# Kernel optimization log

Measured on AMD Instinct MI355X. Metric: run time of the kernel, lower is better.

Reference implementation:

```python
import jax, jax.numpy as jnp
import numpy as np

DIM = 1024
HEADS = 16
HEAD_DIM = DIM // HEADS
T_MAX = 128
V = 12
T = 128
B = 4
N = V * T + 1  # 1537, includes cls token


def setup_inputs() -> dict:
    key = jax.random.key(0)
    ks = jax.random.split(key, 9)
    s = 0.02
    return {
        "x": jax.random.normal(ks[0], (B, N, DIM), dtype=jnp.float32),
        "qkv_w": jax.random.normal(ks[1], (3 * DIM, DIM), dtype=jnp.float32) * s,
        "in_proj_w": jax.random.normal(ks[2], (3 * DIM, DIM), dtype=jnp.float32) * s,
        "in_proj_b": jax.random.normal(ks[3], (3 * DIM,), dtype=jnp.float32) * s,
        "out_proj_w": jax.random.normal(ks[4], (DIM, DIM), dtype=jnp.float32) * s,
        "out_proj_b": jax.random.normal(ks[5], (DIM,), dtype=jnp.float32) * s,
        "proj_w": jax.random.normal(ks[6], (DIM, DIM), dtype=jnp.float32) * s,
        "proj_b": jax.random.normal(ks[7], (DIM,), dtype=jnp.float32) * s,
        "ids_restore": jax.random.randint(ks[8], (B, V * T), 0, 1000000, dtype=jnp.int64),
        "V_input": V,
        "T_input": T,
    }


def _rope_tables(dtype):
    # theta_d = 10000^{-2d/head_dim}, positions 0..T_max (position 0 is the cls slot)
    theta = 10000.0 ** (-jnp.arange(0, HEAD_DIM, 2, dtype=dtype) / HEAD_DIM)  # (hd/2,)
    pos = jnp.arange(1 + T_MAX, dtype=dtype)
    ang = pos[:, None] * theta[None, :]  # (1+T_max, hd/2)
    return jnp.cos(ang), jnp.sin(ang)


def _rotate(t, cos_g, sin_g):
    # t: (B, N, D); cos_g/sin_g: (B, N-1, 1, hd/2) gathered per non-cls token
    b, n, d = t.shape
    t4 = t.reshape(b, n, HEADS, HEAD_DIM)
    re, im = t4[..., ::2], t4[..., 1::2]  # even/odd interleave -> (B,N,H,hd/2)
    # cls token uses position 0: cos=1, sin=0 -> identity rotation, halves concatenated
    cls = jnp.concatenate([re[:, :1], im[:, :1]], axis=-1)  # (B,1,H,hd)
    rest = jnp.concatenate(
        [re[:, 1:] * cos_g - im[:, 1:] * sin_g,
         re[:, 1:] * sin_g + im[:, 1:] * cos_g], axis=-1)  # (B,N-1,H,hd)
    return jnp.concatenate([cls, rest], axis=1).reshape(b, n, d)


def reference(x, qkv_w, in_proj_w, in_proj_b, out_proj_w, out_proj_b,
              proj_w, proj_b, ids_restore, V_input, T_input):
    b, n, d = x.shape
    # --- qkv projection (no bias) ---
    qkv = jnp.einsum('bnd,ed->bne', x, qkv_w)  # (B,N,3D)
    q, k, v = jnp.split(qkv, 3, axis=-1)
    # --- temporal RoPE with ids_restore-based gather ---
    cos_t, sin_t = _rope_tables(x.dtype)  # (1+T_max, hd/2)
    ids_shuffle = jnp.argsort(ids_restore, axis=1)[:, : n - 1] % V_input  # (B,N-1)
    cos_g = cos_t[ids_shuffle + 1][:, :, None, :]  # gather from cos[:,1:] slice
    sin_g = sin_t[ids_shuffle + 1][:, :, None, :]
    q = _rotate(q, cos_g, sin_g)
    k = _rotate(k, cos_g, sin_g)
    # --- nn.MultiheadAttention (batch_first, no mask, eval) ---
    wq, wk, wv = in_proj_w[:d], in_proj_w[d:2 * d], in_proj_w[2 * d:]
    bq, bk, bv = in_proj_b[:d], in_proj_b[d:2 * d], in_proj_b[2 * d:]
    qp = (jnp.einsum('bnd,ed->bne', q, wq) + bq).reshape(b, n, HEADS, HEAD_DIM)
    kp = (jnp.einsum('bnd,ed->bne', k, wk) + bk).reshape(b, n, HEADS, HEAD_DIM)
    vp = (jnp.einsum('bnd,ed->bne', v, wv) + bv).reshape(b, n, HEADS, HEAD_DIM)
    scale = 1.0 / jnp.sqrt(jnp.asarray(HEAD_DIM, x.dtype))
    scores = jnp.einsum('bqhe,bkhe->bhqk', qp * scale, kp)  # (B,H,N,N)
    attn = jax.nn.softmax(scores, axis=-1)
    ctx = jnp.einsum('bhqk,bkhe->bqhe', attn, vp).reshape(b, n, d)
    mha_out = jnp.einsum('bnd,ed->bne', ctx, out_proj_w) + out_proj_b
    # --- final projection ---
    out = jnp.einsum('bnd,ed->bne', mha_out, proj_w) + proj_b
    return out


if __name__ == '__main__':
    inp = setup_inputs()
    print(reference(**inp).shape)
```

## Files before the change

kernel.cpp:

```cpp
#include <hip/hip_runtime.h>
#include <math.h>

#define B_ 4
#define NTOK 1537
#define NH 16
#define NROWS 6148
#define RPAD 6272
#define KDIM 1024
#define NKT 49

typedef __attribute__((ext_vector_type(8))) short short8;
typedef __attribute__((ext_vector_type(4))) float f32x4;
typedef __attribute__((ext_vector_type(16))) float f32x16;
typedef __attribute__((ext_vector_type(4))) unsigned short ushort4v;
typedef __attribute__((ext_vector_type(4))) unsigned int uint4v;
typedef __attribute__((ext_vector_type(2))) unsigned int uint2v;

__device__ __forceinline__ float bf2f(unsigned short u){
  unsigned int x = ((unsigned int)u) << 16;
  return __uint_as_float(x);
}
__device__ __forceinline__ unsigned short f2bf(float f){
  unsigned int x = __float_as_uint(f);
  x += 0x7fff + ((x >> 16) & 1);
  return (unsigned short)(x >> 16);
}
__device__ __forceinline__ unsigned int pack_bf16(float lo, float hi){
  return (unsigned int)f2bf(lo) | ((unsigned int)f2bf(hi) << 16);
}
__device__ __forceinline__ unsigned int pack_bf16_fast(float lo, float hi){
  unsigned int ue = __float_as_uint(lo) + 0x8000u;
  unsigned int uo = __float_as_uint(hi) + 0x8000u;
  return __builtin_amdgcn_perm(uo, ue, 0x07060302u);
}
__device__ __forceinline__ float fast_exp2(float x){
  return __builtin_amdgcn_exp2f(x);
}
__device__ __forceinline__ uint2v permswap(unsigned int a, unsigned int b){
  return __builtin_amdgcn_permlane32_swap(a, b, false, false);
}
__device__ __forceinline__ void gload_lds16(const void* g, void* l){
  __builtin_amdgcn_global_load_lds((const __attribute__((address_space(1))) unsigned int*)g,
                                   (__attribute__((address_space(3))) unsigned int*)l, 16, 0, 0);
}
__device__ __forceinline__ f32x4 mfma16(short8 a, short8 b, f32x4 c){
  return __builtin_amdgcn_mfma_f32_16x16x32_bf16(a, b, c, 0, 0, 0);
}
__device__ __forceinline__ f32x16 mfma32(short8 a, short8 b, f32x16 c){
  return __builtin_amdgcn_mfma_f32_32x32x16_bf16(a, b, c, 0, 0, 0);
}

__global__ __launch_bounds__(256) void cvt_w_kernel(const float* __restrict__ src,
                                                    unsigned short* __restrict__ dst, int n){
  int i = (blockIdx.x*256 + threadIdx.x)*4;
  if (i >= n) return;
  f32x4 v = *(const f32x4*)(src + i);
  ushort4v o;
  #pragma unroll
  for (int j=0;j<4;j++) o[j] = f2bf(v[j]);
  *(ushort4v*)(dst + i) = o;
}

__global__ __launch_bounds__(256) void cvt_wT_kernel(const float* __restrict__ src, int r0,
                                                     unsigned short* __restrict__ dst){
  __shared__ float Tl[64][65];
  int ct = blockIdx.x, rt = blockIdx.y;
  int t = threadIdx.x;
  int i = t >> 4, j4 = (t & 15) * 4;
  #pragma unroll
  for (int s = 0; s < 4; s++){
    int rl = s*16 + i;
    f32x4 v = *(const f32x4*)(src + (size_t)(r0 + rt*64 + rl)*1024 + ct*64 + j4);
    Tl[rl][j4+0]=v[0]; Tl[rl][j4+1]=v[1]; Tl[rl][j4+2]=v[2]; Tl[rl][j4+3]=v[3];
  }
  __syncthreads();
  #pragma unroll
  for (int s = 0; s < 4; s++){
    int cl = s*16 + i;
    ushort4v o;
    #pragma unroll
    for (int k=0;k<4;k++) o[k] = f2bf(Tl[j4+k][cl]);
    *(ushort4v*)(dst + (size_t)(ct*64 + cl)*1024 + rt*64 + j4) = o;
  }
}

__global__ __launch_bounds__(256) void cvt_x_kernel(const float* __restrict__ x,
                                                    unsigned short* __restrict__ xb){
  size_t i = ((size_t)blockIdx.x*256 + threadIdx.x)*4;
  if (i >= (size_t)RPAD*KDIM) return;
  size_t row = i >> 10;
  ushort4v o;
  if (row < NROWS){
    f32x4 v = *(const f32x4*)(x + i);
    #pragma unroll
    for (int j=0;j<4;j++) o[j] = f2bf(v[j]);
  } else {
    o = (ushort4v)0;
  }
  *(ushort4v*)(xb + i) = o;
}

__global__ __launch_bounds__(64) void fuse_bias_kernel(const float* __restrict__ pw,
    const float* __restrict__ opb, const float* __restrict__ pb, float* __restrict__ bf){
  int c = blockIdx.x;
  int t = threadIdx.x;
  const float* row = pw + (size_t)c*1024;
  float s = 0.f;
  #pragma unroll
  for (int e=0; e<16; e++) s += row[t + e*64] * opb[t + e*64];
  #pragma unroll
  for (int off=1; off<64; off<<=1) s += __shfl_xor(s, off);
  if (t == 0) bf[c] = s + pb[c];
}

__global__ void rope_tables_kernel(float* __restrict__ ct, float* __restrict__ st){
  int i = threadIdx.x;
  if (i >= 13*32) return;
  int p = i >> 5, j = i & 31;
  float th = powf(10000.f, -(float)j * (1.f/32.f));
  float ang = (float)p * th;
  ct[i] = cosf(ang);
  st[i] = sinf(ang);
}

__global__ __launch_bounds__(256) void argsort_kernel(const int* __restrict__ ids,
                                                      int* __restrict__ postab){
  __shared__ int vals[1536];
  int b = blockIdx.x;
  const int* src = ids + b*1536;
  for (int i=threadIdx.x; i<1536; i+=256) vals[i] = src[i];
  __syncthreads();
  int i = blockIdx.y*256 + threadIdx.x;
  int v = vals[i];
  int rank = 0;
  for (int j=0;j<1536;j++){
    int u = vals[j];
    rank += (u < v) || (u == v && j < i);
  }
  postab[b*1536 + rank] = (i % 12) + 1;
}

__global__ __launch_bounds__(256) void rope_kernel(unsigned short* __restrict__ qkv,
                                                   const int* __restrict__ postab,
                                                   const float* __restrict__ ct,
                                                   const float* __restrict__ st){
  int idx = blockIdx.x*256 + threadIdx.x;
  if (idx >= B_*NTOK*NH) return;
  int h = idx & 15;
  int bn = idx >> 4;
  int b = bn / NTOK;
  int n = bn - b*NTOK;
  unsigned short* rowp = qkv + (size_t)bn*2048;
  int pos = (n == 0) ? 0 : postab[b*1536 + (n-1)];
  const float* cr = ct + pos*32;
  const float* sr = st + pos*32;
  #pragma unroll
  for (int part=0; part<2; part++){
    unsigned short* p = rowp + part*1024 + h*64;
    uint4v vv[8];
    #pragma unroll
    for (int i=0;i<8;i++) vv[i] = ((const uint4v*)p)[i];
    unsigned short* tp = (unsigned short*)vv;
    unsigned short ov[64];
    if (n == 0){
      #pragma unroll
      for (int j=0;j<32;j++){ ov[j] = tp[2*j]; ov[32+j] = tp[2*j+1]; }
    } else {
      #pragma unroll
      for (int j=0;j<32;j++){
        float re = bf2f(tp[2*j]), im = bf2f(tp[2*j+1]);
        float c = cr[j], s = sr[j];
        ov[j]    = f2bf(re*c - im*s);
        ov[32+j] = f2bf(re*s + im*c);
      }
    }
    #pragma unroll
    for (int i=0;i<8;i++) ((uint4v*)p)[i] = ((const uint4v*)ov)[i];
  }
}

__device__ __forceinline__ void gemm_body(const unsigned short* __restrict__ A, int lda,
    const unsigned short* __restrict__ W,
    const float* __restrict__ bias, float scale,
    unsigned short* __restrict__ outb, float* __restrict__ outf, int ldo, int mvalid,
    int rowBase, int colBase)
{
  __shared__ alignas(16) unsigned short At[128][32];
  __shared__ alignas(16) unsigned short Bt[128][32];
  int t = threadIdx.x, w = t >> 6, lane = t & 63;
  int g = lane >> 4, l15 = lane & 15;
  int rb = (w >> 1) * 64, cb = (w & 1) * 64;
  f32x4 acc[4][4];
  #pragma unroll
  for (int m=0;m<4;m++)
    #pragma unroll
    for (int n=0;n<4;n++) acc[m][n] = 0.f;
  int srow = lane >> 2;
  int scol = (lane & 3) * 8;
  for (int kb = 0; kb < KDIM; kb += 32){
    __syncthreads();
    #pragma unroll
    for (int i=0;i<2;i++){
      int rr = i*64 + w*16 + srow;
      gload_lds16(A + (size_t)(rowBase + rr)*lda + kb + scol, &At[i*64 + w*16][0]);
      gload_lds16(W + (size_t)(colBase + rr)*KDIM + kb + scol, &Bt[i*64 + w*16][0]);
    }
    __syncthreads();
    short8 af[4], bf[4];
    #pragma unroll
    for (int m=0;m<4;m++) af[m] = *(const short8*)&At[rb + m*16 + l15][g*8];
    #pragma unroll
    for (int n=0;n<4;n++) bf[n] = *(const short8*)&Bt[cb + n*16 + l15][g*8];
    #pragma unroll
    for (int m=0;m<4;m++)
      #pragma unroll
      for (int n=0;n<4;n++)
        acc[m][n] = mfma16(af[m], bf[n], acc[m][n]);
  }
  #pragma unroll
  for (int m=0;m<4;m++)
    #pragma unroll
    for (int n=0;n<4;n++){
      int col = colBase + cb + n*16 + l15;
      float bv = bias ? bias[col] : 0.f;
      #pragma unroll
      for (int r=0;r<4;r++){
        int row = rowBase + rb + m*16 + g*4 + r;
        if (row < mvalid){
          float v = (acc[m][n][r] + bv) * scale;
          if (outf) outf[(size_t)row*ldo + col] = v;
          else      outb[(size_t)row*ldo + col] = f2bf(v);
        }
      }
    }
}

__global__ __launch_bounds__(256) void gemm_kernel(const unsigned short* __restrict__ A, int lda,
    const unsigned short* __restrict__ W,
    const float* __restrict__ bias, float scale,
    unsigned short* __restrict__ outb, float* __restrict__ outf, int ldo, int mvalid)
{
  gemm_body(A, lda, W, bias, scale, outb, outf, ldo, mvalid,
            blockIdx.x*128, blockIdx.y*128);
}

__global__ __launch_bounds__(256) void gemm_qkv_kernel(const unsigned short* __restrict__ xb,
    const unsigned short* __restrict__ qkvwb, const unsigned short* __restrict__ Wvb,
    const float* __restrict__ ipb, unsigned short* __restrict__ qkb,
    unsigned short* __restrict__ vpb)
{
  int cy = blockIdx.y;
  bool isV = cy >= 16;
  const unsigned short* W = isV ? Wvb : qkvwb;
  const float* bias = isV ? ipb + 2048 : nullptr;
  unsigned short* outb = isV ? vpb : qkb;
  int ldo = isV ? 1024 : 2048;
  int colBase = (isV ? cy - 16 : cy) * 128;
  gemm_body(xb, 1024, W, bias, 1.f, outb, nullptr, ldo, NROWS,
            blockIdx.x*128, colBase);
}

__global__ __launch_bounds__(256) void gemm_inproj_kernel(const unsigned short* __restrict__ qkb,
    const unsigned short* __restrict__ ipwb, const float* __restrict__ ipb,
    unsigned short* __restrict__ qpb, unsigned short* __restrict__ kpb)
{
  int z = blockIdx.z;
  const unsigned short* A = qkb + z*1024;
  const unsigned short* W = ipwb + (size_t)z*1024*1024;
  const float* bias = ipb + z*1024;
  float scale = (z == 0) ? 0.125f*1.44269504f : 1.f;
  unsigned short* outb = (z == 0) ? qpb : kpb;
  gemm_body(A, 2048, W, bias, scale, outb, nullptr, 1024, NROWS,
            blockIdx.x*128, blockIdx.y*128);
}

__global__ __launch_bounds__(256) void gemm_prep_kernel(const unsigned short* __restrict__ pwb,
    const unsigned short* __restrict__ opwT, const unsigned short* __restrict__ wv,
    const unsigned short* __restrict__ qkvwTv,
    unsigned short* __restrict__ Wfb, unsigned short* __restrict__ Wvb)
{
  int z = blockIdx.z;
  const unsigned short* A = z ? wv : pwb;
  const unsigned short* W = z ? qkvwTv : opwT;
  unsigned short* outb = z ? Wvb : Wfb;
  gemm_body(A, 1024, W, nullptr, 1.f, outb, nullptr, 1024, 1024,
            blockIdx.x*128, blockIdx.y*128);
}

__global__ __launch_bounds__(256) void frag_kernel(const unsigned short* __restrict__ kp,
    const unsigned short* __restrict__ vp,
    unsigned short* __restrict__ kf, unsigned short* __restrict__ vf){
  __shared__ alignas(16) unsigned short Tl[32][72];
  int bh = blockIdx.x, kt = blockIdx.y;
  int b = bh >> 4, h = bh & 15;
  int t = threadIdx.x;
  if (blockIdx.z == 0){
    int lane = t & 63, c = t >> 6;
    int l31 = lane & 31, hh = lane >> 5;
    int key = kt*32 + l31; if (key > NTOK-1) key = NTOK-1;
    uint4v v = *(const uint4v*)(kp + (size_t)(b*NTOK + key)*KDIM + h*64 + c*16 + hh*8);
    *(uint4v*)(kf + (size_t)(bh*NKT + kt)*2048 + c*512 + lane*8) = v;
  } else {
    {
      int r = t >> 3, ch = t & 7;
      int key = kt*32 + r;
      uint4v v;
      if (key < NTOK){
        v = *(const uint4v*)(vp + (size_t)(b*NTOK + key)*KDIM + h*64 + ch*8);
      } else v = (uint4v)0;
      *(uint4v*)&Tl[r][ch*8] = v;
    }
    __syncthreads();
    {
      int lane = t & 63, w = t >> 6;
      int l31 = lane & 31, hh = lane >> 5;
      int dblk = w >> 1, c = w & 1;
      unsigned short ov[8];
      #pragma unroll
      for (int j=0;j<8;j++) ov[j] = Tl[c*16 + hh*8 + j][dblk*32 + l31];
      *(uint4v*)(vf + (size_t)(bh*NKT + kt)*2048 + w*512 + lane*8) = *(const uint4v*)ov;
    }
  }
}

__global__ __launch_bounds__(256) void attn_kernel(const unsigned short* __restrict__ qp,
    const unsigned short* __restrict__ kf, const unsigned short* __restrict__ vf,
    unsigned short* __restrict__ ctx)
{
  int bh = blockIdx.x;
  int qt = blockIdx.y;
  int b = bh >> 4, hd = bh & 15;
  int t = threadIdx.x, w = t >> 6, lane = t & 63;
  int l31 = lane & 31, hh = lane >> 5;
  int qrow = qt*128 + w*32 + l31;
  int qcl = qrow > NTOK-1 ? NTOK-1 : qrow;
  const unsigned short* qb = qp + (((size_t)(b*NTOK + qcl)*NH + hd) << 6) + hh*8;
  short8 qf[4];
  #pragma unroll
  for (int c=0;c<4;c++) qf[c] = *(const short8*)(qb + c*16);
  const unsigned short* kfb = kf + (size_t)(bh*NKT)*2048 + lane*8;
  const unsigned short* vfb = vf + (size_t)(bh*NKT)*2048 + lane*8;
  float m_ = -3e38f, l_ = 0.f;
  f32x16 o0 = 0.f, o1 = 0.f;

  auto soft_pv = [&](f32x16 cc, short8 va00, short8 va01, short8 va10, short8 va11){
    float t0 = fmaxf(fmaxf(cc[0],cc[1]), fmaxf(cc[2],cc[3]));
    float t1 = fmaxf(fmaxf(cc[4],cc[5]), fmaxf(cc[6],cc[7]));
    float t2 = fmaxf(fmaxf(cc[8],cc[9]), fmaxf(cc[10],cc[11]));
    float t3 = fmaxf(fmaxf(cc[12],cc[13]), fmaxf(cc[14],cc[15]));
    float mx = fmaxf(fmaxf(t0,t1), fmaxf(t2,t3));
    {
      uint2v pr = permswap(__float_as_uint(mx), __float_as_uint(mx));
      mx = fmaxf(__uint_as_float(pr[0]), __uint_as_float(pr[1]));
    }
    if (!__all(mx <= m_ + 11.5f)){
      float mn = fmaxf(m_, mx);
      float al = fast_exp2(m_ - mn);
      m_ = mn;
      l_ *= al;
      #pragma unroll
      for (int i=0;i<16;i++){ o0[i] *= al; o1[i] *= al; }
    }
    float p[16], rs = 0.f;
    #pragma unroll
    for (int i=0;i<16;i++){ p[i] = fast_exp2(cc[i] - m_); }
    #pragma unroll
    for (int i=0;i<16;i++) rs += p[i];
    l_ += rs;
    unsigned int W[8];
    #pragma unroll
    for (int wd=0; wd<8; wd++) W[wd] = pack_bf16_fast(p[2*wd], p[2*wd+1]);
    uint2v e0 = permswap(W[0], W[2]);
    uint2v e1 = permswap(W[1], W[3]);
    uint2v e2 = permswap(W[4], W[6]);
    uint2v e3 = permswap(W[5], W[7]);
    uint4v u0, u1;
    u0[0]=e0[0]; u0[1]=e1[0]; u0[2]=e0[1]; u0[3]=e1[1];
    u1[0]=e2[0]; u1[1]=e3[0]; u1[2]=e2[1]; u1[3]=e3[1];
    short8 pb0, pb1;
    __builtin_memcpy(&pb0, &u0, 16);
    __builtin_memcpy(&pb1, &u1, 16);
    o0 = mfma32(va00, pb0, o0);
    o0 = mfma32(va01, pb1, o0);
    o1 = mfma32(va10, pb0, o1);
    o1 = mfma32(va11, pb1, o1);
  };

  short8 ka[4];
  #pragma unroll
  for (int c=0;c<4;c++) ka[c] = *(const short8*)(kfb + c*512);
  f32x16 cc = 0.f;
  cc = mfma32(ka[0], qf[0], cc);
  cc = mfma32(ka[1], qf[1], cc);
  cc = mfma32(ka[2], qf[2], cc);
  cc = mfma32(ka[3], qf[3], cc);
  #pragma unroll
  for (int c=0;c<4;c++) ka[c] = *(const short8*)(kfb + 2048 + c*512);

  for (int kt=0; kt<48; ++kt){
    const unsigned short* vB = vfb + (size_t)kt*2048;
    short8 va00 = *(const short8*)(vB);
    short8 va01 = *(const short8*)(vB + 512);
    short8 va10 = *(const short8*)(vB + 1024);
    short8 va11 = *(const short8*)(vB + 1536);
    f32x16 cn = 0.f;
    cn = mfma32(ka[0], qf[0], cn);
    cn = mfma32(ka[1], qf[1], cn);
    cn = mfma32(ka[2], qf[2], cn);
    cn = mfma32(ka[3], qf[3], cn);
    int ktn = kt+2 < NKT-1 ? kt+2 : NKT-1;
    const unsigned short* kB = kfb + (size_t)ktn*2048;
    #pragma unroll
    for (int c=0;c<4;c++) ka[c] = *(const short8*)(kB + c*512);
    soft_pv(cc, va00, va01, va10, va11);
    cc = cn;
  }
  {
    const unsigned short* vB = vfb + (size_t)48*2048;
    short8 va00 = *(const short8*)(vB);
    short8 va01 = *(const short8*)(vB + 512);
    short8 va10 = *(const short8*)(vB + 1024);
    short8 va11 = *(const short8*)(vB + 1536);
    #pragma unroll
    for (int i=0;i<16;i++) cc[i] = (i == 0 && hh == 0) ? cc[i] : -1e30f;
    soft_pv(cc, va00, va01, va10, va11);
  }
  {
    uint2v pr = permswap(__float_as_uint(l_), __float_as_uint(l_));
    l_ = __uint_as_float(pr[0]) + __uint_as_float(pr[1]);
  }
  if (qrow < NTOK){
    float inv = 1.f / l_;
    unsigned short* cb = ctx + (((size_t)(b*NTOK + qrow)*NH + hd) << 6) + 4*hh;
    #pragma unroll
    for (int s=0;s<4;s++){
      uint2v u;
      u[0] = pack_bf16(o0[4*s]*inv,   o0[4*s+1]*inv);
      u[1] = pack_bf16(o0[4*s+2]*inv, o0[4*s+3]*inv);
      *(uint2v*)(cb + 8*s) = u;
    }
    #pragma unroll
    for (int s=0;s<4;s++){
      uint2v u;
      u[0] = pack_bf16(o1[4*s]*inv,   o1[4*s+1]*inv);
      u[1] = pack_bf16(o1[4*s+2]*inv, o1[4*s+3]*inv);
      *(uint2v*)(cb + 32 + 8*s) = u;
    }
  }
}

extern "C" void kernel_launch(void* const* d_in, const int* in_sizes, int n_in,
                              void* d_out, int out_size, void* d_ws, size_t ws_size,
                              hipStream_t stream)
{
  const float* x    = (const float*)d_in[0];
  const float* qkvw = (const float*)d_in[1];
  const float* ipw  = (const float*)d_in[2];
  const float* ipb  = (const float*)d_in[3];
  const float* opw  = (const float*)d_in[4];
  const float* opb  = (const float*)d_in[5];
  const float* pw   = (const float*)d_in[6];
  const float* pb   = (const float*)d_in[7];
  const int*   ids  = (const int*)d_in[8];
  float* out = (float*)d_out;

  char* p = (char*)d_ws;
  auto alloc = [&](size_t bytes)->char* {
    char* r = p; p += (bytes + 255) & ~(size_t)255; return r;
  };
  unsigned short* xb     = (unsigned short*)alloc((size_t)RPAD*1024*2);
  unsigned short* qkvwb  = (unsigned short*)alloc((size_t)2048*1024*2);
  unsigned short* ipwb   = (unsigned short*)alloc((size_t)3072*1024*2);
  unsigned short* pwb    = (unsigned short*)alloc((size_t)1024*1024*2);
  unsigned short* opwT   = (unsigned short*)alloc((size_t)1024*1024*2);
  unsigned short* qkvwTv = (unsigned short*)alloc((size_t)1024*1024*2);
  unsigned short* Wfb    = (unsigned short*)alloc((size_t)1024*1024*2);
  unsigned short* Wvb    = (unsigned short*)alloc((size_t)1024*1024*2);
  float*          bfb    = (float*)alloc(1024*4);
  unsigned short* qkb    = (unsigned short*)alloc((size_t)RPAD*2048*2);
  unsigned short* qpb    = (unsigned short*)alloc((size_t)RPAD*1024*2);
  unsigned short* kpb    = (unsigned short*)alloc((size_t)RPAD*1024*2);
  unsigned short* vpb    = (unsigned short*)alloc((size_t)RPAD*1024*2);
  unsigned short* ctxb   = (unsigned short*)alloc((size_t)RPAD*1024*2);
  int*   postab = (int*)alloc((size_t)B_*1536*4);
  float* ctab   = (float*)alloc(13*32*4);
  float* stab   = (float*)alloc(13*32*4);
  unsigned short* vfb = xb;
  unsigned short* kfb = qkb;

  cvt_w_kernel<<<2048, 256, 0, stream>>>(qkvw, qkvwb, 2048*1024);
  cvt_w_kernel<<<3072, 256, 0, stream>>>(ipw,  ipwb,  3072*1024);
  cvt_w_kernel<<<1024, 256, 0, stream>>>(pw,   pwb,   1024*1024);
  cvt_wT_kernel<<<dim3(16,16), 256, 0, stream>>>(opw,  0,    opwT);
  cvt_wT_kernel<<<dim3(16,16), 256, 0, stream>>>(qkvw, 2048, qkvwTv);
  cvt_x_kernel<<<RPAD, 256, 0, stream>>>(x, xb);
  rope_tables_kernel<<<1, 512, 0, stream>>>(ctab, stab);
  argsort_kernel<<<dim3(B_, 6), 256, 0, stream>>>(ids, postab);

  gemm_prep_kernel<<<dim3(8, 8, 2), 256, 0, stream>>>(pwb, opwT, ipwb + (size_t)2048*1024,
                                                      qkvwTv, Wfb, Wvb);
  fuse_bias_kernel<<<1024, 64, 0, stream>>>(pw, opb, pb, bfb);

  gemm_qkv_kernel<<<dim3(RPAD/128, 24), 256, 0, stream>>>(xb, qkvwb, Wvb, ipb, qkb, vpb);
  rope_kernel<<<(B_*NTOK*NH + 255)/256, 256, 0, stream>>>(qkb, postab, ctab, stab);
  gemm_inproj_kernel<<<dim3(RPAD/128, 8, 2), 256, 0, stream>>>(qkb, ipwb, ipb, qpb, kpb);
  frag_kernel<<<dim3(B_*NH, NKT, 2), 256, 0, stream>>>(kpb, vpb, kfb, vfb);
  attn_kernel<<<dim3(B_*NH, 13), 256, 0, stream>>>(qpb, kfb, vfb, ctxb);
  gemm_kernel<<<dim3(RPAD/128, 8), 256, 0, stream>>>(ctxb, 1024, Wfb, bfb, 1.f,
                                                     nullptr, out, 1024, NROWS);
}
```

Measured before the change: 369.4 us.

## Double GEMM K-step to 64 with XOR-swizzled LDS and XCD block remapping

The shared GEMM body now stages 64-wide K tiles instead of 32, which halves the number of barrier pairs per output tile. LDS columns are XOR-swizzled by row to avoid bank conflicts on the wider rows. The GEMM kernels also remap block indices so consecutive tiles land on the same XCD, aiming for better L2 reuse of A/W panels. LDS use doubles and the swizzle assumes grid sizes divisible by 8.

```diff
diff --git a/kernel.cpp b/kernel.cpp
--- a/kernel.cpp
+++ b/kernel.cpp
@@ -48,6 +48,14 @@
 }
 __device__ __forceinline__ f32x16 mfma32(short8 a, short8 b, f32x16 c){
   return __builtin_amdgcn_mfma_f32_32x32x16_bf16(a, b, c, 0, 0, 0);
+}
+__device__ __forceinline__ void xcd_swz(int& bx, int& by){
+  int nx = gridDim.x;
+  int lin = blockIdx.y * nx + blockIdx.x;
+  int cpx = (nx * gridDim.y) >> 3;
+  int swz = (lin & 7) * cpx + (lin >> 3);
+  bx = swz % nx;
+  by = swz / nx;
 }
 
 __global__ __launch_bounds__(256) void cvt_w_kernel(const float* __restrict__ src,
@@ -185,8 +193,8 @@
     unsigned short* __restrict__ outb, float* __restrict__ outf, int ldo, int mvalid,
     int rowBase, int colBase)
 {
-  __shared__ alignas(16) unsigned short At[128][32];
-  __shared__ alignas(16) unsigned short Bt[128][32];
+  __shared__ alignas(16) unsigned short At[128][64];
+  __shared__ alignas(16) unsigned short Bt[128][64];
   int t = threadIdx.x, w = t >> 6, lane = t & 63;
   int g = lane >> 4, l15 = lane & 15;
   int rb = (w >> 1) * 64, cb = (w & 1) * 64;
@@ -195,27 +203,32 @@
   for (int m=0;m<4;m++)
     #pragma unroll
     for (int n=0;n<4;n++) acc[m][n] = 0.f;
-  int srow = lane >> 2;
-  int scol = (lane & 3) * 8;
-  for (int kb = 0; kb < KDIM; kb += 32){
+  int srow = lane >> 3;
+  int scol = ((lane & 7) ^ (lane >> 3)) * 8;
+  int rsw = l15 & 7;
+  for (int kb = 0; kb < KDIM; kb += 64){
     __syncthreads();
     #pragma unroll
-    for (int i=0;i<2;i++){
-      int rr = i*64 + w*16 + srow;
-      gload_lds16(A + (size_t)(rowBase + rr)*lda + kb + scol, &At[i*64 + w*16][0]);
-      gload_lds16(W + (size_t)(colBase + rr)*KDIM + kb + scol, &Bt[i*64 + w*16][0]);
+    for (int i=0;i<4;i++){
+      int rr = i*32 + w*8 + srow;
+      gload_lds16(A + (size_t)(rowBase + rr)*lda + kb + scol, &At[i*32 + w*8][0]);
+      gload_lds16(W + (size_t)(colBase + rr)*KDIM + kb + scol, &Bt[i*32 + w*8][0]);
     }
     __syncthreads();
-    short8 af[4], bf[4];
-    #pragma unroll
-    for (int m=0;m<4;m++) af[m] = *(const short8*)&At[rb + m*16 + l15][g*8];
-    #pragma unroll
-    for (int n=0;n<4;n++) bf[n] = *(const short8*)&Bt[cb + n*16 + l15][g*8];
-    #pragma unroll
-    for (int m=0;m<4;m++)
-      #pragma unroll
-      for (int n=0;n<4;n++)
-        acc[m][n] = mfma16(af[m], bf[n], acc[m][n]);
+    #pragma unroll
+    for (int ks=0; ks<2; ks++){
+      int rc = ((ks*4 + g) ^ rsw) * 8;
+      short8 af[4], bf[4];
+      #pragma unroll
+      for (int m=0;m<4;m++) af[m] = *(const short8*)&At[rb + m*16 + l15][rc];
+      #pragma unroll
+      for (int n=0;n<4;n++) bf[n] = *(const short8*)&Bt[cb + n*16 + l15][rc];
+      #pragma unroll
+      for (int m=0;m<4;m++)
+        #pragma unroll
+        for (int n=0;n<4;n++)
+          acc[m][n] = mfma16(af[m], bf[n], acc[m][n]);
+    }
   }
   #pragma unroll
   for (int m=0;m<4;m++)
@@ -240,8 +253,8 @@
     const float* __restrict__ bias, float scale,
     unsigned short* __restrict__ outb, float* __restrict__ outf, int ldo, int mvalid)
 {
-  gemm_body(A, lda, W, bias, scale, outb, outf, ldo, mvalid,
-            blockIdx.x*128, blockIdx.y*128);
+  int bx, by; xcd_swz(bx, by);
+  gemm_body(A, lda, W, bias, scale, outb, outf, ldo, mvalid, bx*128, by*128);
 }
 
 __global__ __launch_bounds__(256) void gemm_qkv_kernel(const unsigned short* __restrict__ xb,
@@ -249,15 +262,14 @@
     const float* __restrict__ ipb, unsigned short* __restrict__ qkb,
     unsigned short* __restrict__ vpb)
 {
-  int cy = blockIdx.y;
-  bool isV = cy >= 16;
+  int bx, by; xcd_swz(bx, by);
+  bool isV = by >= 16;
   const unsigned short* W = isV ? Wvb : qkvwb;
   const float* bias = isV ? ipb + 2048 : nullptr;
   unsigned short* outb = isV ? vpb : qkb;
   int ldo = isV ? 1024 : 2048;
-  int colBase = (isV ? cy - 16 : cy) * 128;
-  gemm_body(xb, 1024, W, bias, 1.f, outb, nullptr, ldo, NROWS,
-            blockIdx.x*128, colBase);
+  int colBase = (isV ? by - 16 : by) * 128;
+  gemm_body(xb, 1024, W, bias, 1.f, outb, nullptr, ldo, NROWS, bx*128, colBase);
 }
 
 __global__ __launch_bounds__(256) void gemm_inproj_kernel(const unsigned short* __restrict__ qkb,
@@ -265,13 +277,13 @@
     unsigned short* __restrict__ qpb, unsigned short* __restrict__ kpb)
 {
   int z = blockIdx.z;
+  int bx, by; xcd_swz(bx, by);
   const unsigned short* A = qkb + z*1024;
   const unsigned short* W = ipwb + (size_t)z*1024*1024;
   const float* bias = ipb + z*1024;
   float scale = (z == 0) ? 0.125f*1.44269504f : 1.f;
   unsigned short* outb = (z == 0) ? qpb : kpb;
-  gemm_body(A, 2048, W, bias, scale, outb, nullptr, 1024, NROWS,
-            blockIdx.x*128, blockIdx.y*128);
+  gemm_body(A, 2048, W, bias, scale, outb, nullptr, 1024, NROWS, bx*128, by*128);
 }
 
 __global__ __launch_bounds__(256) void gemm_prep_kernel(const unsigned short* __restrict__ pwb,
```

New measurement: 363.7 us. Within noise of the previous version (-1.5%).
